# Performance work log

Measured on AMD Instinct MI355X. Metric: run time of the kernel, lower is better.

The kernel has to match this reference:

```python
import jax, jax.numpy as jnp
import numpy as np


def setup_inputs() -> dict:
    key = jax.random.key(0)
    ks = jax.random.split(key, 6)
    N, Tx, Ty = 8, 1024, 128
    enc_dim, dec_dim, Ca = 512, 1024, 128
    sc = 0.02
    return {
        "h": jax.random.normal(ks[0], (N, Tx, enc_dim), jnp.float32),
        "s": jax.random.normal(ks[1], (N, Ty, dec_dim), jnp.float32),
        "Wh": jax.random.normal(ks[2], (enc_dim, Ca), jnp.float32) * sc,
        "Ws": jax.random.normal(ks[3], (dec_dim, Ca), jnp.float32) * sc,
        "b": jax.random.normal(ks[4], (Ca,), jnp.float32) * sc,
        "v": jax.random.normal(ks[5], (Ca,), jnp.float32) * sc,
    }


def reference(h, s, Wh, Ws, b, v):
    # W([h;s]) + b == h@Wh + s@Ws + b (split of the concat Linear weight)
    ph = jnp.einsum("nxc,ca->nxa", h, Wh)            # (N, Tx, Ca)
    ps = jnp.einsum("nyd,da->nya", s, Ws) + b        # (N, Ty, Ca)
    # broadcast-add -> tanh -> dot with v : (N, Ty, Tx)
    e = jnp.einsum("nyxa,a->nyx", jnp.tanh(ps[:, :, None, :] + ph[:, None, :, :]), v)
    return jax.nn.softmax(e, axis=-1)                # attention over Tx
```

## Files before the change

### kernel.cpp

```cpp
#include <hip/hip_runtime.h>
#include <stdint.h>


typedef float  f32x4  __attribute__((ext_vector_type(4)));
typedef __bf16 bf16x8 __attribute__((ext_vector_type(8)));

#define LOG2E     1.4426950408889634f
#define TWO_LOG2E 2.8853900817779268f

__global__ void __launch_bounds__(256) transpose_cast(
    const float* __restrict__ Wh, const float* __restrict__ Ws,
    __bf16* __restrict__ WhT, __bf16* __restrict__ WsT)
{
    int bid = blockIdx.x;
    const float* src; __bf16* dst; int K, c0;
    if (bid < 8) { src = Wh; dst = WhT; K = 512;  c0 = bid * 64; }
    else         { src = Ws; dst = WsT; K = 1024; c0 = (bid - 8) * 64; }
    __shared__ float tile[64][129];
    int t = threadIdx.x;
    for (int i = 0; i < 8192; i += 256) {
        int idx = i + t;
        int r = idx >> 7, col = idx & 127;
        tile[r][col] = src[(size_t)(c0 + r) * 128 + col];
    }
    __syncthreads();
    for (int i = 0; i < 8192; i += 256) {
        int idx = i + t;
        int a = idx >> 6, cc = idx & 63;
        dst[(size_t)a * K + c0 + cc] = (__bf16)tile[cc][a];
    }
}

__global__ void __launch_bounds__(256) gemm_fused(
    const __bf16* __restrict__ WhT, const __bf16* __restrict__ WsT,
    const float* __restrict__ h, const float* __restrict__ s,
    float* __restrict__ Eph, float* __restrict__ Eps,
    const float* __restrict__ bias)
{
    int bid = blockIdx.x;
    int tid = threadIdx.x, lane = tid & 63, w = tid >> 6;
    int mbase = (w & 1) * 64;
    const __bf16* A; const float* B; float* Cp; int K; bool isPs;
    int colg;
    if (bid < 256) {
        isPs = false; A = WhT; B = h; K = 512;
        colg = bid * 32 + (w >> 1) * 16;
        int n = colg >> 10, x = colg & 1023;
        Cp = Eph + (size_t)n * 131072 + x;
    } else {
        isPs = true; A = WsT; B = s; K = 1024;
        colg = (bid - 256) * 32 + (w >> 1) * 16;
        Cp = Eps + colg;
    }
    int q = lane >> 4;
    const float*  Bp = B + (size_t)(colg + (lane & 15)) * K + q * 8;
    const __bf16* Ap = A + (size_t)(mbase + (lane & 15)) * K + q * 8;

    f32x4 acc[4] = {};
    float4 b0 = *(const float4*)(Bp);
    float4 b1 = *(const float4*)(Bp + 4);
    bf16x8 a_[4];
    #pragma unroll
    for (int i = 0; i < 4; ++i) a_[i] = *(const bf16x8*)(Ap + (size_t)i * 16 * K);

    for (int k0 = 0; k0 < K; k0 += 32) {
        int kn = k0 + 32; if (kn > K - 32) kn = K - 32;
        float4 nb0 = *(const float4*)(Bp + kn);
        float4 nb1 = *(const float4*)(Bp + kn + 4);
        bf16x8 na[4];
        #pragma unroll
        for (int i = 0; i < 4; ++i)
            na[i] = *(const bf16x8*)(Ap + (size_t)i * 16 * K + kn);
        bf16x8 bf;
        bf[0] = (__bf16)b0.x; bf[1] = (__bf16)b0.y;
        bf[2] = (__bf16)b0.z; bf[3] = (__bf16)b0.w;
        bf[4] = (__bf16)b1.x; bf[5] = (__bf16)b1.y;
        bf[6] = (__bf16)b1.z; bf[7] = (__bf16)b1.w;
        #pragma unroll
        for (int i = 0; i < 4; ++i)
            acc[i] = __builtin_amdgcn_mfma_f32_16x16x32_bf16(a_[i], bf, acc[i], 0, 0, 0);
        b0 = nb0; b1 = nb1;
        #pragma unroll
        for (int i = 0; i < 4; ++i) a_[i] = na[i];
    }

    int col = lane & 15;
    #pragma unroll
    for (int i = 0; i < 4; ++i) {
        #pragma unroll
        for (int r = 0; r < 4; ++r) {
            int m = mbase + i * 16 + q * 4 + r;
            float vv = acc[i][r];
            if (isPs) vv += bias[m];
            Cp[(size_t)m * 1024 + col] =
                __builtin_amdgcn_exp2f(vv * TWO_LOG2E);
        }
    }
}

__global__ void __launch_bounds__(512) attn_softmax(
    const float* __restrict__ Eph, const float* __restrict__ Eps,
    const float* __restrict__ v, float* __restrict__ out)
{
    int bid = blockIdx.x;
    int n = bid >> 5, yg = bid & 31;
    int ny = n * 128 + yg * 4;
    const float2* ph2 = (const float2*)(Eph + (size_t)n * 131072);
    int t = threadIdx.x;

    __shared__ float4 ps_s[128];
    __shared__ float  v_s[128];
    __shared__ float  wred[4][8];
    __shared__ float  VsumS;

    if (t < 128) {
        ps_s[t] = *(const float4*)(Eps + (size_t)t * 1024 + ny);
        v_s[t]  = v[t];
    } else if (t < 192) {
        int l = t - 128;
        float vv = v[l] + v[l + 64];
        for (int m = 32; m; m >>= 1) vv += __shfl_xor(vv, m);
        if (l == 0) VsumS = vv;
    }
    __syncthreads();
    float Vsum = VsumS;

    float acc0[4] = {0, 0, 0, 0}, acc1[4] = {0, 0, 0, 0};
    #pragma unroll 4
    for (int a = 0; a < 128; ++a) {
        float4 ps4 = ps_s[a];
        float  va  = v_s[a];
        float2 p2  = ph2[a * 512 + t];
        float psy[4] = {ps4.x, ps4.y, ps4.z, ps4.w};
        #pragma unroll
        for (int y = 0; y < 4; ++y) {
            float z0 = fmaf(psy[y], p2.x, 1.f);
            float z1 = fmaf(psy[y], p2.y, 1.f);
            acc0[y] = fmaf(va, __builtin_amdgcn_rcpf(z0), acc0[y]);
            acc1[y] = fmaf(va, __builtin_amdgcn_rcpf(z1), acc1[y]);
        }
    }

    float e0[4], e1[4];
    #pragma unroll
    for (int y = 0; y < 4; ++y) {
        e0[y] = fmaf(-2.f, acc0[y], Vsum);
        e1[y] = fmaf(-2.f, acc1[y], Vsum);
    }

    int lane = t & 63, wv = t >> 6;
    #pragma unroll
    for (int y = 0; y < 4; ++y) {
        float mx = fmaxf(e0[y], e1[y]);
        for (int m = 32; m; m >>= 1) mx = fmaxf(mx, __shfl_xor(mx, m));
        if (lane == 0) wred[y][wv] = mx;
    }
    __syncthreads();
    float mxv[4];
    #pragma unroll
    for (int y = 0; y < 4; ++y) {
        float mx = wred[y][0];
        #pragma unroll
        for (int i = 1; i < 8; ++i) mx = fmaxf(mx, wred[y][i]);
        mxv[y] = mx;
    }
    __syncthreads();
    float s0[4], s1[4], smv[4];
    #pragma unroll
    for (int y = 0; y < 4; ++y) {
        s0[y] = __builtin_amdgcn_exp2f((e0[y] - mxv[y]) * LOG2E);
        s1[y] = __builtin_amdgcn_exp2f((e1[y] - mxv[y]) * LOG2E);
        float sm = s0[y] + s1[y];
        for (int m = 32; m; m >>= 1) sm += __shfl_xor(sm, m);
        if (lane == 0) wred[y][wv] = sm;
    }
    __syncthreads();
    #pragma unroll
    for (int y = 0; y < 4; ++y) {
        float sm = 0.f;
        #pragma unroll
        for (int i = 0; i < 8; ++i) sm += wred[y][i];
        smv[y] = __builtin_amdgcn_rcpf(sm);
    }
    #pragma unroll
    for (int y = 0; y < 4; ++y) {
        float2 o; o.x = s0[y] * smv[y]; o.y = s1[y] * smv[y];
        ((float2*)(out + (size_t)(ny + y) * 1024))[t] = o;
    }
}

extern "C" void kernel_launch(void* const* d_in, const int* in_sizes, int n_in,
                              void* d_out, int out_size, void* d_ws, size_t ws_size,
                              hipStream_t stream) {
    const float* h  = (const float*)d_in[0];
    const float* s  = (const float*)d_in[1];
    const float* Wh = (const float*)d_in[2];
    const float* Ws = (const float*)d_in[3];
    const float* b  = (const float*)d_in[4];
    const float* v  = (const float*)d_in[5];
    float* out = (float*)d_out;

    char* ws = (char*)d_ws;
    float*  Eph = (float*)ws;
    float*  Eps = (float*)(ws + (4u << 20));
    __bf16* WhT = (__bf16*)(ws + (4u << 20) + (512u << 10));
    __bf16* WsT = WhT + (size_t)128 * 512;

    transpose_cast<<<24, 256, 0, stream>>>(Wh, Ws, WhT, WsT);
    gemm_fused<<<288, 256, 0, stream>>>(WhT, WsT, h, s, Eph, Eps, b);
    attn_softmax<<<256, 512, 0, stream>>>(Eph, Eps, v, out);
}
```

Before: 134.1 us.

## Combine four reciprocal terms into one rcp with packed FMA in attention kernel

```diff
diff --git a/kernel.cpp b/kernel.cpp
--- a/kernel.cpp
+++ b/kernel.cpp
@@ -3,10 +3,12 @@
 
 
 typedef float  f32x4  __attribute__((ext_vector_type(4)));
+typedef float  f32x2  __attribute__((ext_vector_type(2)));
 typedef __bf16 bf16x8 __attribute__((ext_vector_type(8)));
 
 #define LOG2E     1.4426950408889634f
 #define TWO_LOG2E 2.8853900817779268f
+#define FMA2(a, b, c) __builtin_elementwise_fma((a), (b), (c))
 
 __global__ void __launch_bounds__(256) transpose_cast(
     const float* __restrict__ Wh, const float* __restrict__ Ws,
@@ -98,26 +100,25 @@
     }
 }
 
-__global__ void __launch_bounds__(512) attn_softmax(
+__global__ void __launch_bounds__(1024) attn_softmax(
     const float* __restrict__ Eph, const float* __restrict__ Eps,
     const float* __restrict__ v, float* __restrict__ out)
 {
     int bid = blockIdx.x;
     int n = bid >> 5, yg = bid & 31;
     int ny = n * 128 + yg * 4;
-    const float2* ph2 = (const float2*)(Eph + (size_t)n * 131072);
+    const float* ph = Eph + (size_t)n * 131072;
     int t = threadIdx.x;
 
     __shared__ float4 ps_s[128];
-    __shared__ float  v_s[128];
-    __shared__ float  wred[4][8];
-    __shared__ float  VsumS;
-
-    if (t < 128) {
-        ps_s[t] = *(const float4*)(Eps + (size_t)t * 1024 + ny);
-        v_s[t]  = v[t];
-    } else if (t < 192) {
-        int l = t - 128;
+    __shared__ float4 v4_s[32];
+    __shared__ float wred[4][16];
+    __shared__ float VsumS;
+
+    if (t < 128) ps_s[t] = *(const float4*)(Eps + (size_t)t * 1024 + ny);
+    if (t >= 128 && t < 160) v4_s[t - 128] = *(const float4*)(v + (t - 128) * 4);
+    if (t >= 960) {
+        int l = t - 960;
         float vv = v[l] + v[l + 64];
         for (int m = 32; m; m >>= 1) vv += __shfl_xor(vv, m);
         if (l == 0) VsumS = vv;
@@ -125,33 +126,51 @@
     __syncthreads();
     float Vsum = VsumS;
 
-    float acc0[4] = {0, 0, 0, 0}, acc1[4] = {0, 0, 0, 0};
-    #pragma unroll 4
-    for (int a = 0; a < 128; ++a) {
-        float4 ps4 = ps_s[a];
-        float  va  = v_s[a];
-        float2 p2  = ph2[a * 512 + t];
-        float psy[4] = {ps4.x, ps4.y, ps4.z, ps4.w};
-        #pragma unroll
-        for (int y = 0; y < 4; ++y) {
-            float z0 = fmaf(psy[y], p2.x, 1.f);
-            float z1 = fmaf(psy[y], p2.y, 1.f);
-            acc0[y] = fmaf(va, __builtin_amdgcn_rcpf(z0), acc0[y]);
-            acc1[y] = fmaf(va, __builtin_amdgcn_rcpf(z1), acc1[y]);
-        }
-    }
-
-    float e0[4], e1[4];
-    #pragma unroll
-    for (int y = 0; y < 4; ++y) {
-        e0[y] = fmaf(-2.f, acc0[y], Vsum);
-        e1[y] = fmaf(-2.f, acc1[y], Vsum);
+    f32x2 acc[2] = {{0.f, 0.f}, {0.f, 0.f}};
+    const f32x2 one2 = {1.f, 1.f};
+    #pragma unroll 2
+    for (int a = 0; a < 128; a += 4) {
+        float4 q0 = ps_s[a + 0], q1 = ps_s[a + 1];
+        float4 q2 = ps_s[a + 2], q3 = ps_s[a + 3];
+        float4 v4 = v4_s[a >> 2];
+        float p0 = ph[(a + 0) * 1024 + t];
+        float p1 = ph[(a + 1) * 1024 + t];
+        float p2 = ph[(a + 2) * 1024 + t];
+        float p3 = ph[(a + 3) * 1024 + t];
+        auto comb2 = [&](f32x2 ey0, f32x2 ey1, f32x2 ey2, f32x2 ey3,
+                         f32x2& ac) {
+            f32x2 w0 = FMA2(ey0, (f32x2)p0, one2);
+            f32x2 w1 = FMA2(ey1, (f32x2)p1, one2);
+            f32x2 w2 = FMA2(ey2, (f32x2)p2, one2);
+            f32x2 w3 = FMA2(ey3, (f32x2)p3, one2);
+            f32x2 d01 = w0 * w1, d23 = w2 * w3;
+            f32x2 n01 = FMA2((f32x2)v4.y, w0, (f32x2)v4.x * w1);
+            f32x2 n23 = FMA2((f32x2)v4.w, w2, (f32x2)v4.z * w3);
+            f32x2 dd = d01 * d23;
+            f32x2 nn = FMA2(n23, d01, n01 * d23);
+            f32x2 r;
+            r.x = __builtin_amdgcn_rcpf(dd.x);
+            r.y = __builtin_amdgcn_rcpf(dd.y);
+            ac = FMA2(nn, r, ac);
+        };
+        f32x2 a01_0 = {q0.x, q0.y}, a01_1 = {q1.x, q1.y};
+        f32x2 a01_2 = {q2.x, q2.y}, a01_3 = {q3.x, q3.y};
+        f32x2 a23_0 = {q0.z, q0.w}, a23_1 = {q1.z, q1.w};
+        f32x2 a23_2 = {q2.z, q2.w}, a23_3 = {q3.z, q3.w};
+        comb2(a01_0, a01_1, a01_2, a01_3, acc[0]);
+        comb2(a23_0, a23_1, a23_2, a23_3, acc[1]);
+    }
+    float e[4];
+    {
+        f32x2 e01 = FMA2((f32x2)(-2.f), acc[0], (f32x2)Vsum);
+        f32x2 e23 = FMA2((f32x2)(-2.f), acc[1], (f32x2)Vsum);
+        e[0] = e01.x; e[1] = e01.y; e[2] = e23.x; e[3] = e23.y;
     }
 
     int lane = t & 63, wv = t >> 6;
     #pragma unroll
     for (int y = 0; y < 4; ++y) {
-        float mx = fmaxf(e0[y], e1[y]);
+        float mx = e[y];
         for (int m = 32; m; m >>= 1) mx = fmaxf(mx, __shfl_xor(mx, m));
         if (lane == 0) wred[y][wv] = mx;
     }
@@ -161,16 +180,15 @@
     for (int y = 0; y < 4; ++y) {
         float mx = wred[y][0];
         #pragma unroll
-        for (int i = 1; i < 8; ++i) mx = fmaxf(mx, wred[y][i]);
+        for (int i = 1; i < 16; ++i) mx = fmaxf(mx, wred[y][i]);
         mxv[y] = mx;
     }
     __syncthreads();
-    float s0[4], s1[4], smv[4];
-    #pragma unroll
-    for (int y = 0; y < 4; ++y) {
-        s0[y] = __builtin_amdgcn_exp2f((e0[y] - mxv[y]) * LOG2E);
-        s1[y] = __builtin_amdgcn_exp2f((e1[y] - mxv[y]) * LOG2E);
-        float sm = s0[y] + s1[y];
+    float sv[4];
+    #pragma unroll
+    for (int y = 0; y < 4; ++y) {
+        sv[y] = __builtin_amdgcn_exp2f((e[y] - mxv[y]) * LOG2E);
+        float sm = sv[y];
         for (int m = 32; m; m >>= 1) sm += __shfl_xor(sm, m);
         if (lane == 0) wred[y][wv] = sm;
     }
@@ -179,13 +197,9 @@
     for (int y = 0; y < 4; ++y) {
         float sm = 0.f;
         #pragma unroll
-        for (int i = 0; i < 8; ++i) sm += wred[y][i];
-        smv[y] = __builtin_amdgcn_rcpf(sm);
-    }
-    #pragma unroll
-    for (int y = 0; y < 4; ++y) {
-        float2 o; o.x = s0[y] * smv[y]; o.y = s1[y] * smv[y];
-        ((float2*)(out + (size_t)(ny + y) * 1024))[t] = o;
+        for (int i = 0; i < 16; ++i) sm += wred[y][i];
+        float r = __builtin_amdgcn_rcpf(sm);
+        out[(size_t)(ny + y) * 1024 + t] = sv[y] * r;
     }
 }
 
@@ -208,5 +222,5 @@
 
     transpose_cast<<<24, 256, 0, stream>>>(Wh, Ws, WhT, WsT);
     gemm_fused<<<288, 256, 0, stream>>>(WhT, WsT, h, s, Eph, Eps, b);
-    attn_softmax<<<256, 512, 0, stream>>>(Eph, Eps, v, out);
-}
+    attn_softmax<<<256, 1024, 0, stream>>>(Eph, Eps, v, out);
+}
```

Result: faster. 130.0 us (-3.1%).
